# Performance work log

Hardware: AMD Instinct MI355X
Metric: run time of the kernel (lower is better)

Reference implementation:

```python
import jax, jax.numpy as jnp
import numpy as np

K = 2  # top-k experts per token


def setup_inputs() -> dict:
    key = jax.random.key(0)
    k1, k2, k3, k4 = jax.random.split(key, 4)
    B, S, D, E = 4, 4096, 1024, 64
    x = jax.random.normal(k1, (B, S, D), dtype=jnp.float32)
    gate_w = jax.random.normal(k2, (E, D), dtype=jnp.float32) * (1.0 / np.sqrt(D))
    noise_weight = jax.random.normal(k3, (E,), dtype=jnp.float32) * 0.02
    noise = jax.random.normal(k4, (B, S, E), dtype=jnp.float32)  # randn_like(logits) * noisy_std(=1.0)
    return {"x": x, "gate_w": gate_w, "noise_weight": noise_weight, "noise": noise}


def reference(x, gate_w, noise_weight, noise):
    E = gate_w.shape[0]
    # logits = x @ W^T  -> [B, S, E]
    logits = jnp.einsum("bsd,ed->bse", x, gate_w)
    logits_noisy = logits + noise * noise_weight  # noisy_std = 1.0 folded into `noise`
    top_vals, top_idx = jax.lax.top_k(logits_noisy, K)  # [B,S,K]
    # scatter top-k logits into a -inf mask, then softmax over experts
    keep = jax.nn.one_hot(top_idx, E, dtype=jnp.bool_).any(axis=-2)  # [B,S,E]
    neg_inf = jnp.finfo(logits_noisy.dtype).min
    sparse = jnp.where(keep, logits_noisy, neg_inf)
    weights = jax.nn.softmax(sparse, axis=-1)
    return weights, top_idx
```

## Files before the change

kernel.cpp:

```cpp
#include <hip/hip_runtime.h>
#include <math.h>


#define DDIM 1024
#define NEXP 64
#define NTOK 16384
#define NSPLIT 8
#define CPB 2
#define CHUNK_SH 12288

typedef float f4 __attribute__((ext_vector_type(4)));
typedef short s8 __attribute__((ext_vector_type(8)));
typedef unsigned int u32;

static __device__ __forceinline__ void split3(float f, short& h, short& m, short& l) {
    const u32 uf = __float_as_uint(f);
    h = (short)(uf >> 16);
    const float r1 = f - __uint_as_float(uf & 0xffff0000u);
    const u32 u1 = __float_as_uint(r1);
    m = (short)(u1 >> 16);
    const float r2 = r1 - __uint_as_float(u1 & 0xffff0000u);
    l = (short)(__float_as_uint(r2) >> 16);
}

static __device__ __forceinline__ void gl_lds16(const void* g, void* l) {
    __builtin_amdgcn_global_load_lds(
        (const __attribute__((address_space(1))) u32*)g,
        (__attribute__((address_space(3))) u32*)l, 16, 0, 0);
}

__global__ __launch_bounds__(256)
void w_prep(const float* __restrict__ gw, short* __restrict__ wimg) {
    const int uid = blockIdx.x * 256 + threadIdx.x;
    const int c   = uid >> 9;
    const int kk  = (uid >> 8) & 1;
    const int e   = (uid >> 2) & 63;
    const int q   = uid & 3;
    const int k0  = c * 64 + kk * 32 + q * 8;
    const float* src = gw + (size_t)e * DDIM + k0;
    s8 hv, mv, lv;
    #pragma unroll
    for (int j = 0; j < 8; ++j) {
        short h, m, l;
        split3(src[j], h, m, l);
        hv[j] = h; mv[j] = m; lv[j] = l;
    }
    const size_t base = (size_t)c * 1536 + (kk * 3) * 256
                      + (e >> 4) * 64 + q * 16 + (e & 15);
    *(s8*)(wimg + (base      ) * 8) = hv;
    *(s8*)(wimg + (base + 256) * 8) = mv;
    *(s8*)(wimg + (base + 512) * 8) = lv;
}

__global__ __launch_bounds__(256, 3)
void gemm_partial(const float* __restrict__ x,
                  const short* __restrict__ wimg,
                  float* __restrict__ part)
{
    __shared__ short bs[CPB * CHUNK_SH];

    const int tid   = threadIdx.x;
    const int lane  = tid & 63;
    const int wv    = tid >> 6;
    const int m     = lane & 15;
    const int q     = lane >> 4;
    const int tile  = blockIdx.x & 255;
    const int split = blockIdx.x >> 8;
    const int tokBase = tile * 64 + wv * 16;

    const short* bsrc = wimg + (size_t)(split * CPB) * CHUNK_SH;
    #pragma unroll
    for (int i = 0; i < 12; ++i) {
        const int off = (wv * 12 + i) * 512;
        gl_lds16(bsrc + off + lane * 8, &bs[off]);
    }

    const float* xrow = x + (size_t)(tokBase + m) * DDIM
                      + split * (CPB * 64) + q * 8;
    f4 A[8];
    #pragma unroll
    for (int cc = 0; cc < CPB; ++cc) {
        A[cc * 4 + 0] = *(const f4*)(xrow + cc * 64);
        A[cc * 4 + 1] = *(const f4*)(xrow + cc * 64 + 4);
        A[cc * 4 + 2] = *(const f4*)(xrow + cc * 64 + 32);
        A[cc * 4 + 3] = *(const f4*)(xrow + cc * 64 + 36);
    }

    f4 acc0[4], acc1[4];
    #pragma unroll
    for (int t = 0; t < 4; ++t) { acc0[t] = (f4)0.f; acc1[t] = (f4)0.f; }

    __syncthreads();

    #pragma unroll
    for (int cc = 0; cc < CPB; ++cc) {
        s8 ah[2], am[2], al[2];
        const float* sv = (const float*)&A[cc * 4];
        #pragma unroll
        for (int kk = 0; kk < 2; ++kk)
            #pragma unroll
            for (int j = 0; j < 8; ++j) {
                short h, mm, l;
                split3(sv[kk * 8 + j], h, mm, l);
                ah[kk][j] = h; am[kk][j] = mm; al[kk][j] = l;
            }

        #pragma unroll
        for (int kk = 0; kk < 2; ++kk) {
            #pragma unroll
            for (int t = 0; t < 4; ++t) {
                const int pb = cc * 1536 + (kk * 3) * 256 + t * 64 + lane;
                const s8 bh = *(const s8*)&bs[(size_t)(pb      ) * 8];
                const s8 bm = *(const s8*)&bs[(size_t)(pb + 256) * 8];
                const s8 bl = *(const s8*)&bs[(size_t)(pb + 512) * 8];
                acc0[t] = __builtin_amdgcn_mfma_f32_16x16x32_bf16(ah[kk], bh, acc0[t], 0, 0, 0);
                acc1[t] = __builtin_amdgcn_mfma_f32_16x16x32_bf16(ah[kk], bm, acc1[t], 0, 0, 0);
                acc1[t] = __builtin_amdgcn_mfma_f32_16x16x32_bf16(am[kk], bh, acc1[t], 0, 0, 0);
                acc1[t] = __builtin_amdgcn_mfma_f32_16x16x32_bf16(ah[kk], bl, acc1[t], 0, 0, 0);
                acc1[t] = __builtin_amdgcn_mfma_f32_16x16x32_bf16(am[kk], bm, acc1[t], 0, 0, 0);
                acc1[t] = __builtin_amdgcn_mfma_f32_16x16x32_bf16(al[kk], bh, acc1[t], 0, 0, 0);
            }
        }
    }

    #pragma unroll
    for (int t = 0; t < 4; ++t)
        #pragma unroll
        for (int r = 0; r < 4; ++r)
            part[((size_t)split * NTOK + tokBase + q * 4 + r) * NEXP + m + 16 * t]
                = acc0[t][r] + acc1[t][r];
}

__global__ __launch_bounds__(256)
void reduce_topk(const float* __restrict__ part,
                 const float* __restrict__ noise_weight,
                 const float* __restrict__ noise,
                 float* __restrict__ out_w,
                 float* __restrict__ out_i)
{
    const int lane  = threadIdx.x & 63;
    const int wv    = threadIdx.x >> 6;
    const int token = blockIdx.x * 4 + wv;

    float sum = 0.f;
    #pragma unroll
    for (int s = 0; s < NSPLIT; ++s)
        sum += part[((size_t)s * NTOK + token) * NEXP + lane];

    const float ln = fmaf(noise[(size_t)token * NEXP + lane], noise_weight[lane], sum);

    float v1 = ln; int i1 = lane;
    #pragma unroll
    for (int off = 32; off > 0; off >>= 1) {
        const float vo = __shfl_xor(v1, off, 64);
        const int   io = __shfl_xor(i1, off, 64);
        if (vo > v1 || (vo == v1 && io < i1)) { v1 = vo; i1 = io; }
    }
    float v2 = (lane == i1) ? -3.4e38f : ln; int i2 = lane;
    #pragma unroll
    for (int off = 32; off > 0; off >>= 1) {
        const float vo = __shfl_xor(v2, off, 64);
        const int   io = __shfl_xor(i2, off, 64);
        if (vo > v2 || (vo == v2 && io < i2)) { v2 = vo; i2 = io; }
    }

    const float d   = expf(v2 - v1);
    const float inv = 1.f / (1.f + d);
    const float wgt = (lane == i1) ? inv : ((lane == i2) ? d * inv : 0.f);
    out_w[(size_t)token * NEXP + lane] = wgt;
    if (lane == 0) {
        out_i[(size_t)token * 2]     = (float)i1;
        out_i[(size_t)token * 2 + 1] = (float)i2;
    }
}

extern "C" void kernel_launch(void* const* d_in, const int* in_sizes, int n_in,
                              void* d_out, int out_size, void* d_ws, size_t ws_size,
                              hipStream_t stream) {
    const float* x     = (const float*)d_in[0];
    const float* gw    = (const float*)d_in[1];
    const float* nwt   = (const float*)d_in[2];
    const float* noise = (const float*)d_in[3];
    float* out_w = (float*)d_out;
    float* out_i = (float*)d_out + (size_t)NTOK * NEXP;

    short* wimg = (short*)d_ws;
    float* part = (float*)((char*)d_ws + 512 * 1024);

    hipLaunchKernelGGL(w_prep, dim3(32), dim3(256), 0, stream, gw, wimg);
    hipLaunchKernelGGL(gemm_partial, dim3(256 * NSPLIT), dim3(256), 0, stream,
                       x, wimg, part);
    hipLaunchKernelGGL(reduce_topk, dim3(NTOK / 4), dim3(256), 0, stream,
                       part, nwt, noise, out_w, out_i);
}
```

Before: 124.9 us.

## Process two 16-token M tiles per wave to reuse LDS weight fragments

Each wave now handles 32 tokens (two 16-row MFMA tiles) instead of 16, so every B fragment read from LDS feeds twice as many MFMAs, and the grid is halved to 1024 blocks. The x loads for the second K chunk are issued as a prefetch while the first chunk is being split into bf16 parts. This cuts LDS reads and the per-block weight staging cost, but doubles accumulator and A-fragment register use, which may lower occupancy under the launch bound of 3 and leaves fewer blocks to spread across CUs.

```diff
diff --git a/kernel.cpp b/kernel.cpp
--- a/kernel.cpp
+++ b/kernel.cpp
@@ -64,9 +64,9 @@
     const int wv    = tid >> 6;
     const int m     = lane & 15;
     const int q     = lane >> 4;
-    const int tile  = blockIdx.x & 255;
-    const int split = blockIdx.x >> 8;
-    const int tokBase = tile * 64 + wv * 16;
+    const int tile  = blockIdx.x & 127;
+    const int split = blockIdx.x >> 7;
+    const int tokBase = tile * 128 + wv * 32;
 
     const short* bsrc = wimg + (size_t)(split * CPB) * CHUNK_SH;
     #pragma unroll
@@ -75,35 +75,52 @@
         gl_lds16(bsrc + off + lane * 8, &bs[off]);
     }
 
-    const float* xrow = x + (size_t)(tokBase + m) * DDIM
-                      + split * (CPB * 64) + q * 8;
-    f4 A[8];
+    const float* xr0 = x + (size_t)(tokBase + m) * DDIM + split * (CPB * 64) + q * 8;
+    const float* xr1 = xr0 + 16 * DDIM;
+
+    f4 stage[2][4];
+    stage[0][0] = *(const f4*)(xr0);
+    stage[0][1] = *(const f4*)(xr0 + 4);
+    stage[0][2] = *(const f4*)(xr0 + 32);
+    stage[0][3] = *(const f4*)(xr0 + 36);
+    stage[1][0] = *(const f4*)(xr1);
+    stage[1][1] = *(const f4*)(xr1 + 4);
+    stage[1][2] = *(const f4*)(xr1 + 32);
+    stage[1][3] = *(const f4*)(xr1 + 36);
+
+    f4 acc0[2][4], acc1[2][4];
+    #pragma unroll
+    for (int mt = 0; mt < 2; ++mt)
+        #pragma unroll
+        for (int t = 0; t < 4; ++t) { acc0[mt][t] = (f4)0.f; acc1[mt][t] = (f4)0.f; }
+
+    __syncthreads();
+
     #pragma unroll
     for (int cc = 0; cc < CPB; ++cc) {
-        A[cc * 4 + 0] = *(const f4*)(xrow + cc * 64);
-        A[cc * 4 + 1] = *(const f4*)(xrow + cc * 64 + 4);
-        A[cc * 4 + 2] = *(const f4*)(xrow + cc * 64 + 32);
-        A[cc * 4 + 3] = *(const f4*)(xrow + cc * 64 + 36);
-    }
-
-    f4 acc0[4], acc1[4];
-    #pragma unroll
-    for (int t = 0; t < 4; ++t) { acc0[t] = (f4)0.f; acc1[t] = (f4)0.f; }
-
-    __syncthreads();
-
-    #pragma unroll
-    for (int cc = 0; cc < CPB; ++cc) {
-        s8 ah[2], am[2], al[2];
-        const float* sv = (const float*)&A[cc * 4];
-        #pragma unroll
-        for (int kk = 0; kk < 2; ++kk)
+        s8 ah[2][2], am[2][2], al[2][2];
+        #pragma unroll
+        for (int mt = 0; mt < 2; ++mt) {
+            const float* sv = (const float*)&stage[mt][0];
             #pragma unroll
-            for (int j = 0; j < 8; ++j) {
-                short h, mm, l;
-                split3(sv[kk * 8 + j], h, mm, l);
-                ah[kk][j] = h; am[kk][j] = mm; al[kk][j] = l;
-            }
+            for (int kk = 0; kk < 2; ++kk)
+                #pragma unroll
+                for (int j = 0; j < 8; ++j) {
+                    short h, mm, l;
+                    split3(sv[kk * 8 + j], h, mm, l);
+                    ah[mt][kk][j] = h; am[mt][kk][j] = mm; al[mt][kk][j] = l;
+                }
+        }
+        if (cc + 1 < CPB) {
+            stage[0][0] = *(const f4*)(xr0 + 64);
+            stage[0][1] = *(const f4*)(xr0 + 68);
+            stage[0][2] = *(const f4*)(xr0 + 96);
+            stage[0][3] = *(const f4*)(xr0 + 100);
+            stage[1][0] = *(const f4*)(xr1 + 64);
+            stage[1][1] = *(const f4*)(xr1 + 68);
+            stage[1][2] = *(const f4*)(xr1 + 96);
+            stage[1][3] = *(const f4*)(xr1 + 100);
+        }
 
         #pragma unroll
         for (int kk = 0; kk < 2; ++kk) {
@@ -113,22 +130,27 @@
                 const s8 bh = *(const s8*)&bs[(size_t)(pb      ) * 8];
                 const s8 bm = *(const s8*)&bs[(size_t)(pb + 256) * 8];
                 const s8 bl = *(const s8*)&bs[(size_t)(pb + 512) * 8];
-                acc0[t] = __builtin_amdgcn_mfma_f32_16x16x32_bf16(ah[kk], bh, acc0[t], 0, 0, 0);
-                acc1[t] = __builtin_amdgcn_mfma_f32_16x16x32_bf16(ah[kk], bm, acc1[t], 0, 0, 0);
-                acc1[t] = __builtin_amdgcn_mfma_f32_16x16x32_bf16(am[kk], bh, acc1[t], 0, 0, 0);
-                acc1[t] = __builtin_amdgcn_mfma_f32_16x16x32_bf16(ah[kk], bl, acc1[t], 0, 0, 0);
-                acc1[t] = __builtin_amdgcn_mfma_f32_16x16x32_bf16(am[kk], bm, acc1[t], 0, 0, 0);
-                acc1[t] = __builtin_amdgcn_mfma_f32_16x16x32_bf16(al[kk], bh, acc1[t], 0, 0, 0);
+                #pragma unroll
+                for (int mt = 0; mt < 2; ++mt) {
+                    acc0[mt][t] = __builtin_amdgcn_mfma_f32_16x16x32_bf16(ah[mt][kk], bh, acc0[mt][t], 0, 0, 0);
+                    acc1[mt][t] = __builtin_amdgcn_mfma_f32_16x16x32_bf16(ah[mt][kk], bm, acc1[mt][t], 0, 0, 0);
+                    acc1[mt][t] = __builtin_amdgcn_mfma_f32_16x16x32_bf16(am[mt][kk], bh, acc1[mt][t], 0, 0, 0);
+                    acc1[mt][t] = __builtin_amdgcn_mfma_f32_16x16x32_bf16(ah[mt][kk], bl, acc1[mt][t], 0, 0, 0);
+                    acc1[mt][t] = __builtin_amdgcn_mfma_f32_16x16x32_bf16(am[mt][kk], bm, acc1[mt][t], 0, 0, 0);
+                    acc1[mt][t] = __builtin_amdgcn_mfma_f32_16x16x32_bf16(al[mt][kk], bh, acc1[mt][t], 0, 0, 0);
+                }
             }
         }
     }
 
     #pragma unroll
-    for (int t = 0; t < 4; ++t)
-        #pragma unroll
-        for (int r = 0; r < 4; ++r)
-            part[((size_t)split * NTOK + tokBase + q * 4 + r) * NEXP + m + 16 * t]
-                = acc0[t][r] + acc1[t][r];
+    for (int mt = 0; mt < 2; ++mt)
+        #pragma unroll
+        for (int t = 0; t < 4; ++t)
+            #pragma unroll
+            for (int r = 0; r < 4; ++r)
+                part[((size_t)split * NTOK + tokBase + mt * 16 + q * 4 + r) * NEXP + m + 16 * t]
+                    = acc0[mt][t][r] + acc1[mt][t][r];
 }
 
 __global__ __launch_bounds__(256)
@@ -188,7 +210,7 @@
     float* part = (float*)((char*)d_ws + 512 * 1024);
 
     hipLaunchKernelGGL(w_prep, dim3(32), dim3(256), 0, stream, gw, wimg);
-    hipLaunchKernelGGL(gemm_partial, dim3(256 * NSPLIT), dim3(256), 0, stream,
+    hipLaunchKernelGGL(gemm_partial, dim3(128 * NSPLIT), dim3(256), 0, stream,
                        x, wimg, part);
     hipLaunchKernelGGL(reduce_topk, dim3(NTOK / 4), dim3(256), 0, stream,
                        part, nwt, noise, out_w, out_i);
```

New measurement: 125.6 us. About the same (+0.6%).
